# Optimization experiments

Measured on AMD Instinct MI355X. Metric: run time of the kernel, lower is better.

## Reference

```python
import jax, jax.numpy as jnp
import numpy as np

E = 512       # embed_dim
H = 8         # num_heads
DH = E // H   # head dim
F = 2048      # dim_feedforward
KS = 33       # NATTEN kernel_size (dilation=1)
NCLS = 1
B = 2
L = 4096      # local tokens (total seq = L + NCLS)
EPS = 1e-5


def layernorm(x, g, b):
    mu = jnp.mean(x, axis=-1, keepdims=True)
    var = jnp.mean(jnp.square(x - mu), axis=-1, keepdims=True)
    return (x - mu) * jax.lax.rsqrt(var + EPS) * g + b


def natten_1d(x, qkv_w, qkv_b, proj_w, proj_b):
    # Neighborhood attention 1D, dilation=1, non-causal, no rel-pos bias.
    b, l, e = x.shape
    qkv = x @ qkv_w.T + qkv_b                       # [b, l, 3E]
    q, k, v = jnp.split(qkv, 3, axis=-1)
    q = q.reshape(b, l, H, DH) * (DH ** -0.5)
    k = k.reshape(b, l, H, DH)
    v = v.reshape(b, l, H, DH)
    # NATTEN window: centered, shifted at edges to keep exactly KS in-bounds neighbors
    starts = jnp.clip(jnp.arange(l) - KS // 2, 0, l - KS)   # [l]
    idx = starts[:, None] + jnp.arange(KS)                  # [l, KS]
    kn = k[:, idx]                                          # [b, l, KS, H, DH]
    vn = v[:, idx]                                          # [b, l, KS, H, DH]
    attn = jnp.einsum('blhd,blkhd->bhlk', q, kn)
    attn = jax.nn.softmax(attn, axis=-1)
    out = jnp.einsum('bhlk,blkhd->blhd', attn, vn).reshape(b, l, e)
    return out @ proj_w.T + proj_b


def global_mha(q_in, kv_in, in_w, in_b, out_w, out_b):
    # torch nn.MultiheadAttention, batch_first, no masks
    bq, lq, e = q_in.shape
    lk = kv_in.shape[1]
    wq, wk, wv = jnp.split(in_w, 3, axis=0)
    bqp, bkp, bvp = jnp.split(in_b, 3, axis=0)
    q = (q_in @ wq.T + bqp).reshape(bq, lq, H, DH) * (DH ** -0.5)
    k = (kv_in @ wk.T + bkp).reshape(bq, lk, H, DH)
    v = (kv_in @ wv.T + bvp).reshape(bq, lk, H, DH)
    attn = jax.nn.softmax(jnp.einsum('bqhd,bkhd->bhqk', q, k), axis=-1)
    out = jnp.einsum('bhqk,bkhd->bqhd', attn, v).reshape(bq, lq, e)
    return out @ out_w.T + out_b


def setup_inputs() -> dict:
    key = jax.random.key(0)
    ks = jax.random.split(key, 16)
    s = 0.02
    return {
        'x': jax.random.normal(ks[0], (B, L + NCLS, E), jnp.float32),
        'ln1_g': jnp.ones((E,), jnp.float32),
        'ln1_b': jnp.zeros((E,), jnp.float32),
        'qkv_w': jax.random.normal(ks[1], (3 * E, E), jnp.float32) * s,
        'qkv_b': jnp.zeros((3 * E,), jnp.float32),
        'na_proj_w': jax.random.normal(ks[2], (E, E), jnp.float32) * s,
        'na_proj_b': jnp.zeros((E,), jnp.float32),
        'in_proj_w': jax.random.normal(ks[3], (3 * E, E), jnp.float32) * s,
        'in_proj_b': jnp.zeros((3 * E,), jnp.float32),
        'out_w': jax.random.normal(ks[4], (E, E), jnp.float32) * s,
        'out_b': jnp.zeros((E,), jnp.float32),
        'ln2_g': jnp.ones((E,), jnp.float32),
        'ln2_b': jnp.zeros((E,), jnp.float32),
        'fc1_w': jax.random.normal(ks[5], (F, E), jnp.float32) * s,
        'fc1_b': jnp.zeros((F,), jnp.float32),
        'fc2_w': jax.random.normal(ks[6], (E, F), jnp.float32) * s,
        'fc2_b': jnp.zeros((E,), jnp.float32),
    }


def reference(x, ln1_g, ln1_b, qkv_w, qkv_b, na_proj_w, na_proj_b,
              in_proj_w, in_proj_b, out_w, out_b, ln2_g, ln2_b,
              fc1_w, fc1_b, fc2_w, fc2_b):
    res = x
    xn = layernorm(x, ln1_g, ln1_b)
    x_local = natten_1d(xn[:, :-NCLS, :], qkv_w, qkv_b, na_proj_w, na_proj_b)
    tmp_key = jnp.concatenate([x_local, xn[:, -NCLS:, :]], axis=1)
    x_cls = global_mha(xn[:, -NCLS:, :], tmp_key, in_proj_w, in_proj_b, out_w, out_b)
    x = res + jnp.concatenate([x_local, x_cls], axis=1)
    res = x
    xn = layernorm(x, ln2_g, ln2_b)
    h = jax.nn.silu(xn @ fc1_w.T + fc1_b)
    return res + (h @ fc2_w.T + fc2_b)
```

## Files before the change

kernel.cpp:

```cpp
#include <hip/hip_runtime.h>
#include <hip/hip_bf16.h>
#include <cstdint>
#include <cstddef>

#define E    512
#define H    8
#define DHD  64
#define FDIM 2048
#define KS   33
#define BB   2
#define LL   4096
#define LP1  4097
#define NTOK 8194
#define NLOC 8192

typedef unsigned short ushort_t;
typedef __bf16 bf16x8_t __attribute__((ext_vector_type(8)));
typedef float  f32x4_t  __attribute__((ext_vector_type(4)));

__device__ __forceinline__ float b2f(unsigned short h) {
  union { unsigned int u; float f; } un; un.u = ((unsigned int)h) << 16; return un.f;
}
__device__ __forceinline__ unsigned short f2b(float f) {
  union { float f; unsigned int u; } un; un.f = f;
  unsigned int u = un.u;
  return (unsigned short)((u + 0x7FFFu + ((u >> 16) & 1u)) >> 16);
}

__device__ __forceinline__ void gload16(const ushort_t* g, ushort_t* l) {
  __builtin_amdgcn_global_load_lds(
      (const __attribute__((address_space(1))) void*)g,
      (__attribute__((address_space(3))) void*)l,
      16, 0, 0);
}

__device__ __forceinline__ int xcd_remap(int hw, int n) {
  int xcd = hw & 7, j = hw >> 3;
  int q = n >> 3, r = n & 7;
  return (xcd < r ? xcd * (q + 1) : r * (q + 1) + (xcd - r) * q) + j;
}

template<int BNT, int WC, int ACT, int OUTF, int ADDRES, int INRM, int OUTRM, int PARTIAL>
__global__ __launch_bounds__(256) void gemm_bt(
    const ushort_t* __restrict__ A, const ushort_t* __restrict__ W,
    const float* __restrict__ bias, float* __restrict__ outF,
    ushort_t* __restrict__ outB, const float* __restrict__ res,
    int M, int N, int K, int klen, int ny, int nz, size_t pstr)
{
  constexpr int MF = 4;
  constexpr int NF = BNT / (WC * 16);
  constexpr int BR = (BNT * 64) / (8 * 256);
  __shared__ ushort_t Alds[128 * 64];
  __shared__ ushort_t Blds[BNT * 64];
  const int t    = threadIdx.x;
  const int lane = t & 63;
  const int w    = t >> 6;
  const int wr   = w / WC, wc = w % WC;

  const int Lid = xcd_remap(blockIdx.x, gridDim.x);
  const int bx  = Lid / (ny * nz);
  const int rem = Lid % (ny * nz);
  const int z   = rem / ny;
  const int by  = rem % ny;
  const int bmBase = bx * 128;
  const int bnBase = by * BNT;
  const int kbeg = z * klen;

  f32x4_t zero = {0.f, 0.f, 0.f, 0.f};
  f32x4_t acc[MF][NF];
  #pragma unroll
  for (int m = 0; m < MF; ++m)
    #pragma unroll
    for (int n = 0; n < NF; ++n) acc[m][n] = zero;

  const int srow = t >> 3;
  const int jsw8 = ((t & 7) ^ (srow & 7)) * 8;
  int arow[4];
  #pragma unroll
  for (int r = 0; r < 4; ++r) {
    int rr = bmBase + r * 32 + srow;
    if (INRM) rr += rr >> 12;
    else if (rr >= M) rr = M - 1;
    arow[r] = rr;
  }
  int brow[BR];
  #pragma unroll
  for (int r = 0; r < BR; ++r) brow[r] = bnBase + r * 32 + srow;

  const int frow = lane & 15;
  const int g    = lane >> 4;

  for (int k0 = kbeg; k0 < kbeg + klen; k0 += 64) {
    #pragma unroll
    for (int r = 0; r < 4; ++r)
      gload16(A + (size_t)arow[r] * K + k0 + jsw8, &Alds[(size_t)(r * 256 + t) * 8]);
    #pragma unroll
    for (int r = 0; r < BR; ++r)
      gload16(W + (size_t)brow[r] * K + k0 + jsw8, &Blds[(size_t)(r * 256 + t) * 8]);
    __syncthreads();
    #pragma unroll
    for (int kk2 = 0; kk2 < 2; ++kk2) {
      bf16x8_t af[MF], bfv[NF];
      const int kosw = ((kk2 * 4 + g) ^ (frow & 7)) << 4;
      #pragma unroll
      for (int m = 0; m < MF; ++m) {
        int row = wr * 64 + m * 16 + frow;
        af[m] = *reinterpret_cast<const bf16x8_t*>((char*)Alds + row * 128 + kosw);
      }
      #pragma unroll
      for (int n = 0; n < NF; ++n) {
        int row = wc * (BNT / WC) + n * 16 + frow;
        bfv[n] = *reinterpret_cast<const bf16x8_t*>((char*)Blds + row * 128 + kosw);
      }
      __builtin_amdgcn_s_setprio(1);
      #pragma unroll
      for (int m = 0; m < MF; ++m)
        #pragma unroll
        for (int n = 0; n < NF; ++n)
          acc[m][n] = __builtin_amdgcn_mfma_f32_16x16x32_bf16(af[m], bfv[n], acc[m][n], 0, 0, 0);
      __builtin_amdgcn_s_setprio(0);
    }
    __syncthreads();
  }

  const int rbase = g * 4;
  const int cbase = frow;
  float* po = nullptr;
  if (PARTIAL) po = (z == nz - 1) ? (float*)outB : outF + (size_t)z * pstr;
  #pragma unroll
  for (int m = 0; m < MF; ++m) {
    #pragma unroll
    for (int r = 0; r < 4; ++r) {
      int gr = bmBase + wr * 64 + m * 16 + rbase + r;
      if (gr < M) {
        int orow = OUTRM ? gr + (gr >> 12) : gr;
        #pragma unroll
        for (int n = 0; n < NF; ++n) {
          int gc = bnBase + wc * (BNT / WC) + n * 16 + cbase;
          float v = acc[m][n][r];
          if (PARTIAL) {
            po[(size_t)orow * N + gc] = v;
          } else {
            v += bias[gc];
            if (ACT == 1) v = v / (1.f + __expf(-v));
            if (ADDRES) v += res[(size_t)gr * N + gc];
            if (OUTF) outF[(size_t)orow * N + gc] = v;
            else      outB[(size_t)orow * N + gc] = f2b(v);
          }
        }
      }
    }
  }
}

template<int NP>
__global__ __launch_bounds__(256) void fc2_reduce(
    float* __restrict__ out, const float* __restrict__ parts, size_t pstr4,
    const float* __restrict__ bias, const float* __restrict__ xa)
{
  size_t i = (size_t)blockIdx.x * 256 + threadIdx.x;
  float4 o = reinterpret_cast<const float4*>(out)[i];
  float4 x = reinterpret_cast<const float4*>(xa)[i];
  float4 bcol = reinterpret_cast<const float4*>(bias)[i & 127];
  o.x += x.x + bcol.x; o.y += x.y + bcol.y;
  o.z += x.z + bcol.z; o.w += x.w + bcol.w;
  #pragma unroll
  for (int zp = 0; zp < NP - 1; ++zp) {
    float4 a = reinterpret_cast<const float4*>(parts)[zp * pstr4 + i];
    o.x += a.x; o.y += a.y; o.z += a.z; o.w += a.w;
  }
  reinterpret_cast<float4*>(out)[i] = o;
}

__global__ __launch_bounds__(256) void ln_fused1(
    const float* __restrict__ x, const float* __restrict__ g,
    const float* __restrict__ be, ushort_t* __restrict__ xn,
    ushort_t* __restrict__ tmpk)
{
  __shared__ float sh[4];
  const int row = blockIdx.x;
  const int t = threadIdx.x;
  const float* xr = x + (size_t)row * E;
  float v0 = xr[t], v1 = xr[t + 256];
  float sum = v0 + v1;
  #pragma unroll
  for (int o = 32; o; o >>= 1) sum += __shfl_xor(sum, o);
  if ((t & 63) == 0) sh[t >> 6] = sum;
  __syncthreads();
  float mean = (sh[0] + sh[1] + sh[2] + sh[3]) * (1.f / E);
  __syncthreads();
  float d0 = v0 - mean, d1 = v1 - mean;
  float vs = d0 * d0 + d1 * d1;
  #pragma unroll
  for (int o = 32; o; o >>= 1) vs += __shfl_xor(vs, o);
  if ((t & 63) == 0) sh[t >> 6] = vs;
  __syncthreads();
  float var = (sh[0] + sh[1] + sh[2] + sh[3]) * (1.f / E);
  float rstd = rsqrtf(var + 1e-5f);
  unsigned short o0 = f2b(d0 * rstd * g[t] + be[t]);
  unsigned short o1 = f2b(d1 * rstd * g[t + 256] + be[t + 256]);
  xn[(size_t)row * E + t] = o0;
  xn[(size_t)row * E + t + 256] = o1;
  if ((row % LP1) == LL) {
    tmpk[(size_t)row * E + t] = o0;
    tmpk[(size_t)row * E + t + 256] = o1;
  }
}

__global__ __launch_bounds__(256) void resid_ln2(
    const float* __restrict__ x, const ushort_t* __restrict__ tmpk,
    const float* __restrict__ xcls, const float* __restrict__ g,
    const float* __restrict__ be, float* __restrict__ xa,
    ushort_t* __restrict__ xn2)
{
  __shared__ float sh[4];
  const int row = blockIdx.x;
  const int b = row / LP1, l = row % LP1;
  const int t = threadIdx.x;
  float a0, a1;
  if (l < LL) { a0 = b2f(tmpk[(size_t)row * E + t]); a1 = b2f(tmpk[(size_t)row * E + t + 256]); }
  else        { a0 = xcls[b * E + t];                a1 = xcls[b * E + t + 256]; }
  float v0 = x[(size_t)row * E + t] + a0;
  float v1 = x[(size_t)row * E + t + 256] + a1;
  xa[(size_t)row * E + t] = v0;
  xa[(size_t)row * E + t + 256] = v1;
  float sum = v0 + v1;
  #pragma unroll
  for (int o = 32; o; o >>= 1) sum += __shfl_xor(sum, o);
  if ((t & 63) == 0) sh[t >> 6] = sum;
  __syncthreads();
  float mean = (sh[0] + sh[1] + sh[2] + sh[3]) * (1.f / E);
  __syncthreads();
  float d0 = v0 - mean, d1 = v1 - mean;
  float vs = d0 * d0 + d1 * d1;
  #pragma unroll
  for (int o = 32; o; o >>= 1) vs += __shfl_xor(vs, o);
  if ((t & 63) == 0) sh[t >> 6] = vs;
  __syncthreads();
  float var = (sh[0] + sh[1] + sh[2] + sh[3]) * (1.f / E);
  float rstd = rsqrtf(var + 1e-5f);
  xn2[(size_t)row * E + t]       = f2b(d0 * rstd * g[t] + be[t]);
  xn2[(size_t)row * E + t + 256] = f2b(d1 * rstd * g[t + 256] + be[t + 256]);
}

__global__ __launch_bounds__(256) void natten_mfma(
    const ushort_t* __restrict__ qkv, ushort_t* __restrict__ out)
{
  __shared__ ushort_t KP[4][64 * 64];
  __shared__ ushort_t VT[4][64 * 72];
  const int w    = threadIdx.x >> 6;
  const int lane = threadIdx.x & 63;
  const int task = blockIdx.x * 4 + w;
  const int h  = task & 7;
  const int qb = (task >> 3) & 127;
  const int b  = task >> 10;
  const int l0 = qb * 32;
  const int kb = l0 - 16;
  const ushort_t* base = qkv + (size_t)b * LL * (3 * E);
  ushort_t* Klds = KP[w];
  ushort_t* Vt   = VT[w];

  {
    const int rsub = lane >> 3;
    const int d0   = (lane & 7) * 8;
    #pragma unroll
    for (int i = 0; i < 8; ++i) {
      int row = i * 8 + rsub;
      int gl = kb + row; gl = gl < 0 ? 0 : (gl > LL - 1 ? LL - 1 : gl);
      bf16x8_t kv = *reinterpret_cast<const bf16x8_t*>(
          base + (size_t)gl * (3 * E) + E + h * 64 + d0);
      int ba = (row * 128 + d0 * 2) ^ ((row & 7) << 4);
      *reinterpret_cast<bf16x8_t*>((char*)Klds + ba) = kv;
    }
  }
  {
    const int a  = lane & 7;
    const int c8 = lane >> 3;
    unsigned int* Vt32 = (unsigned int*)Vt;
    #pragma unroll
    for (int i = 0; i < 4; ++i) {
      int rp = i * 8 + c8;
      int g0 = kb + rp * 2;     g0 = g0 < 0 ? 0 : (g0 > LL - 1 ? LL - 1 : g0);
      int g1 = kb + rp * 2 + 1; g1 = g1 < 0 ? 0 : (g1 > LL - 1 ? LL - 1 : g1);
      const ushort_t* v0 = base + (size_t)g0 * (3 * E) + 2 * E + h * 64 + a * 8;
      const ushort_t* v1 = base + (size_t)g1 * (3 * E) + 2 * E + h * 64 + a * 8;
      ushort4 x0 = *(const ushort4*)v0,       x1 = *(const ushort4*)v1;
      ushort4 y0 = *(const ushort4*)(v0 + 4), y1 = *(const ushort4*)(v1 + 4);
      int d = a * 8;
      Vt32[(d + 0) * 36 + rp] = (unsigned)x0.x | ((unsigned)x1.x << 16);
      Vt32[(d + 1) * 36 + rp] = (unsigned)x0.y | ((unsigned)x1.y << 16);
      Vt32[(d + 2) * 36 + rp] = (unsigned)x0.z | ((unsigned)x1.z << 16);
      Vt32[(d + 3) * 36 + rp] = (unsigned)x0.w | ((unsigned)x1.w << 16);
      Vt32[(d + 4) * 36 + rp] = (unsigned)y0.x | ((unsigned)y1.x << 16);
      Vt32[(d + 5) * 36 + rp] = (unsigned)y0.y | ((unsigned)y1.y << 16);
      Vt32[(d + 6) * 36 + rp] = (unsigned)y0.z | ((unsigned)y1.z << 16);
      Vt32[(d + 7) * 36 + rp] = (unsigned)y0.w | ((unsigned)y1.w << 16);
    }
  }

  const int p = lane & 15, g = lane >> 4;
  bf16x8_t qf[2][2];
  #pragma unroll
  for (int mt = 0; mt < 2; ++mt)
    #pragma unroll
    for (int ks = 0; ks < 2; ++ks)
      qf[mt][ks] = *reinterpret_cast<const bf16x8_t*>(
          base + (size_t)(l0 + mt * 16 + p) * (3 * E) + h * 64 + ks * 32 + g * 8);

  f32x4_t zero = {0.f, 0.f, 0.f, 0.f};
  f32x4_t accS[2][4];
  #pragma unroll
  for (int mt = 0; mt < 2; ++mt)
    #pragma unroll
    for (int nt = 0; nt < 4; ++nt) accS[mt][nt] = zero;
  #pragma unroll
  for (int ks = 0; ks < 2; ++ks) {
    bf16x8_t kf[4];
    #pragma unroll
    for (int nt = 0; nt < 4; ++nt) {
      int row = nt * 16 + p;
      int ba = (row * 128 + (ks * 32 + g * 8) * 2) ^ ((row & 7) << 4);
      kf[nt] = *reinterpret_cast<const bf16x8_t*>((char*)Klds + ba);
    }
    #pragma unroll
    for (int mt = 0; mt < 2; ++mt)
      #pragma unroll
      for (int nt = 0; nt < 4; ++nt)
        accS[mt][nt] = __builtin_amdgcn_mfma_f32_16x16x32_bf16(qf[mt][ks], kf[nt], accS[mt][nt], 0, 0, 0);
  }

  ushort_t* Plds = Klds;
  #pragma unroll
  for (int mt = 0; mt < 2; ++mt) {
    #pragma unroll
    for (int r = 0; r < 4; ++r) {
      int lq = l0 + mt * 16 + g * 4 + r;
      int st = lq - 16; st = st < 0 ? 0 : (st > LL - KS ? LL - KS : st);
      int clo = st - kb, chi = clo + 32;
      float sv[4];
      float mx = -1e30f;
      #pragma unroll
      for (int nt = 0; nt < 4; ++nt) {
        int c = nt * 16 + p;
        float s = accS[mt][nt][r] * 0.125f;
        s = (c >= clo && c <= chi) ? s : -1e30f;
        sv[nt] = s;
        mx = fmaxf(mx, s);
      }
      mx = fmaxf(mx, __shfl_xor(mx, 1));
      mx = fmaxf(mx, __shfl_xor(mx, 2));
      mx = fmaxf(mx, __shfl_xor(mx, 4));
      mx = fmaxf(mx, __shfl_xor(mx, 8));
      float sum = 0.f;
      #pragma unroll
      for (int nt = 0; nt < 4; ++nt) { float e = __expf(sv[nt] - mx); sv[nt] = e; sum += e; }
      sum += __shfl_xor(sum, 1);
      sum += __shfl_xor(sum, 2);
      sum += __shfl_xor(sum, 4);
      sum += __shfl_xor(sum, 8);
      float inv = 1.f / sum;
      int q = mt * 16 + g * 4 + r;
      #pragma unroll
      for (int nt = 0; nt < 4; ++nt)
        Plds[q * 72 + nt * 16 + p] = f2b(sv[nt] * inv);
    }
  }

  f32x4_t accO[2][4];
  #pragma unroll
  for (int mt = 0; mt < 2; ++mt)
    #pragma unroll
    for (int nt = 0; nt < 4; ++nt) accO[mt][nt] = zero;
  #pragma unroll
  for (int ks = 0; ks < 2; ++ks) {
    bf16x8_t pf[2], vf[4];
    #pragma unroll
    for (int mt = 0; mt < 2; ++mt)
      pf[mt] = *reinterpret_cast<const bf16x8_t*>(
          (char*)Plds + (mt * 16 + p) * 144 + (ks * 32 + g * 8) * 2);
    #pragma unroll
    for (int nt = 0; nt < 4; ++nt)
      vf[nt] = *reinterpret_cast<const bf16x8_t*>(
          (char*)Vt + (nt * 16 + p) * 144 + (ks * 32 + g * 8) * 2);
    #pragma unroll
    for (int mt = 0; mt < 2; ++mt)
      #pragma unroll
      for (int nt = 0; nt < 4; ++nt)
        accO[mt][nt] = __builtin_amdgcn_mfma_f32_16x16x32_bf16(pf[mt], vf[nt], accO[mt][nt], 0, 0, 0);
  }

  #pragma unroll
  for (int mt = 0; mt < 2; ++mt) {
    #pragma unroll
    for (int r = 0; r < 4; ++r) {
      int lq = l0 + mt * 16 + g * 4 + r;
      ushort_t* orow = out + ((size_t)(b * LL) + lq) * E + h * 64;
      #pragma unroll
      for (int nt = 0; nt < 4; ++nt)
        orow[nt * 16 + p] = f2b(accO[mt][nt][r]);
    }
  }
}

__global__ __launch_bounds__(256) void qcls_kernel(
    const ushort_t* __restrict__ xn, const float* __restrict__ inw,
    const float* __restrict__ inb, float* __restrict__ qcls)
{
  int i = blockIdx.x * 256 + threadIdx.x;
  int b = i >> 9, d = i & 511;
  const ushort_t* xr = xn + ((size_t)b * LP1 + LL) * E;
  const float* wr = inw + (size_t)d * E;
  float s = 0.f;
  for (int e = 0; e < E; e += 4) {
    ushort4 xv = *reinterpret_cast<const ushort4*>(xr + e);
    s += b2f(xv.x) * wr[e] + b2f(xv.y) * wr[e + 1] + b2f(xv.z) * wr[e + 2] + b2f(xv.w) * wr[e + 3];
  }
  qcls[i] = (s + inb[d]) * 0.125f;
}

__global__ __launch_bounds__(256) void gscore_kernel(
    const float* __restrict__ qcls, const ushort_t* __restrict__ kv,
    float* __restrict__ sc)
{
  const int wav = blockIdx.x * 4 + (threadIdx.x >> 6);
  if (wav >= BB * LP1) return;
  const int lane = threadIdx.x & 63;
  const int b = wav / LP1, j = wav % LP1;
  const ushort_t* kr = kv + (size_t)wav * 1024 + lane * 8;
  const float* q = qcls + b * E + lane * 8;
  ushort4 ka = *reinterpret_cast<const ushort4*>(kr);
  ushort4 kb4 = *reinterpret_cast<const ushort4*>(kr + 4);
  float s = b2f(ka.x) * q[0] + b2f(ka.y) * q[1] + b2f(ka.z) * q[2] + b2f(ka.w) * q[3]
          + b2f(kb4.x) * q[4] + b2f(kb4.y) * q[5] + b2f(kb4.z) * q[6] + b2f(kb4.w) * q[7];
  s += __shfl_xor(s, 1); s += __shfl_xor(s, 2); s += __shfl_xor(s, 4);
  if ((lane & 7) == 0) sc[((size_t)(b * 8) + (lane >> 3)) * LP1 + j] = s;
}

__global__ __launch_bounds__(256) void gsoftmax_kernel(float* __restrict__ sc)
{
  float* row = sc + (size_t)blockIdx.x * LP1;
  __shared__ float sh[4];
  const int t = threadIdx.x;
  float m = -1e30f;
  for (int i = t; i < LP1; i += 256) m = fmaxf(m, row[i]);
  #pragma unroll
  for (int o = 32; o; o >>= 1) m = fmaxf(m, __shfl_xor(m, o));
  if ((t & 63) == 0) sh[t >> 6] = m;
  __syncthreads();
  m = fmaxf(fmaxf(sh[0], sh[1]), fmaxf(sh[2], sh[3]));
  __syncthreads();
  float s = 0.f;
  for (int i = t; i < LP1; i += 256) { float e = __expf(row[i] - m); row[i] = e; s += e; }
  #pragma unroll
  for (int o = 32; o; o >>= 1) s += __shfl_xor(s, o);
  if ((t & 63) == 0) sh[t >> 6] = s;
  __syncthreads();
  float inv = 1.f / (sh[0] + sh[1] + sh[2] + sh[3]);
  for (int i = t; i < LP1; i += 256) row[i] *= inv;
}

__global__ __launch_bounds__(256) void gpv_kernel(
    const float* __restrict__ sc, const ushort_t* __restrict__ kv,
    float* __restrict__ parts)
{
  __shared__ float red[4][64];
  const int bh = blockIdx.y;
  const int b = bh >> 3, h = bh & 7;
  const int c = blockIdx.x;
  const int lane = threadIdx.x & 63, s4 = threadIdx.x >> 6;
  const int j0 = c * 512;
  const int jend = (j0 + 512 < LP1) ? j0 + 512 : LP1;
  const float* prow = sc + (size_t)bh * LP1;
  const ushort_t* vbase = kv + (size_t)b * LP1 * 1024 + 512 + h * 64 + lane;
  float acc = 0.f;
  for (int j = j0 + s4; j < jend; j += 4)
    acc += prow[j] * b2f(vbase[(size_t)j * 1024]);
  red[s4][lane] = acc;
  __syncthreads();
  if (s4 == 0)
    parts[((size_t)c * 16 + bh) * 64 + lane] = red[0][lane] + red[1][lane] + red[2][lane] + red[3][lane];
}

__global__ void gpv_reduce(const float* __restrict__ parts, float* __restrict__ oc)
{
  int i = blockIdx.x * 256 + threadIdx.x;
  if (i < BB * E) {
    float s = 0.f;
    #pragma unroll
    for (int c = 0; c < 9; ++c) s += parts[c * 1024 + i];
    oc[i] = s;
  }
}

__global__ __launch_bounds__(256) void xcls_kernel(
    const float* __restrict__ oc, const float* __restrict__ ow,
    const float* __restrict__ ob, float* __restrict__ xc)
{
  int i = blockIdx.x * 256 + threadIdx.x;
  if (i >= BB * E) return;
  int b = i >> 9, n = i & 511;
  const float* o = oc + b * E;
  const float* wr = ow + (size_t)n * E;
  float s = ob[n];
  for (int m = 0; m < E; ++m) s += o[m] * wr[m];
  xc[i] = s;
}

__global__ void cvt_all(
    const float* __restrict__ s0, ushort_t* __restrict__ d0, int n0,
    const float* __restrict__ s1, ushort_t* __restrict__ d1, int n1,
    const float* __restrict__ s2, ushort_t* __restrict__ d2, int n2,
    const float* __restrict__ s3, ushort_t* __restrict__ d3, int n3,
    const float* __restrict__ s4, ushort_t* __restrict__ d4, int n4)
{
  int i = (blockIdx.x * 256 + threadIdx.x) * 4;
  const float* s; ushort_t* d;
  if (i < n0)                { s = s0; d = d0; }
  else if ((i -= n0) < n1)   { s = s1; d = d1; }
  else if ((i -= n1) < n2)   { s = s2; d = d2; }
  else if ((i -= n2) < n3)   { s = s3; d = d3; }
  else if ((i -= n3) < n4)   { s = s4; d = d4; }
  else return;
  float4 v = *reinterpret_cast<const float4*>(s + i);
  ushort4 o;
  o.x = f2b(v.x); o.y = f2b(v.y); o.z = f2b(v.z); o.w = f2b(v.w);
  *reinterpret_cast<ushort4*>(d + i) = o;
}

extern "C" void kernel_launch(void* const* d_in, const int* in_sizes, int n_in,
                              void* d_out, int out_size, void* d_ws, size_t ws_size,
                              hipStream_t stream)
{
  const float* x      = (const float*)d_in[0];
  const float* ln1_g  = (const float*)d_in[1];
  const float* ln1_b  = (const float*)d_in[2];
  const float* qkv_w  = (const float*)d_in[3];
  const float* qkv_b  = (const float*)d_in[4];
  const float* na_w   = (const float*)d_in[5];
  const float* na_b   = (const float*)d_in[6];
  const float* in_w   = (const float*)d_in[7];
  const float* in_b   = (const float*)d_in[8];
  const float* out_w  = (const float*)d_in[9];
  const float* out_b  = (const float*)d_in[10];
  const float* ln2_g  = (const float*)d_in[11];
  const float* ln2_b  = (const float*)d_in[12];
  const float* fc1_w  = (const float*)d_in[13];
  const float* fc1_b  = (const float*)d_in[14];
  const float* fc2_w  = (const float*)d_in[15];
  const float* fc2_b  = (const float*)d_in[16];
  float* out = (float*)d_out;

  char* pws = (char*)d_ws;
  size_t off = 0;
  auto alloc = [&](size_t bytes) {
    void* r = pws + off; off = (off + bytes + 255) & ~(size_t)255; return r;
  };
  ushort_t* w_qkv = (ushort_t*)alloc((size_t)3 * E * E * 2);
  ushort_t* w_na  = (ushort_t*)alloc((size_t)E * E * 2);
  ushort_t* w_in  = (ushort_t*)alloc((size_t)3 * E * E * 2);
  ushort_t* w_fc1 = (ushort_t*)alloc((size_t)FDIM * E * 2);
  ushort_t* w_fc2 = (ushort_t*)alloc((size_t)E * FDIM * 2);
  ushort_t* xn1   = (ushort_t*)alloc((size_t)NTOK * E * 2);
  char*     bigR  = (char*)alloc((size_t)NTOK * FDIM * 2);
  ushort_t* qkvb  = (ushort_t*)bigR;
  ushort_t* natt  = (ushort_t*)(bigR + (size_t)NLOC * 3 * E * 2);
  ushort_t* kvg   = (ushort_t*)bigR;
  ushort_t* hbuf  = (ushort_t*)bigR;
  ushort_t* tmpk  = (ushort_t*)alloc((size_t)NTOK * E * 2);
  float*    sc    = (float*)alloc((size_t)BB * H * LP1 * 4);
  float*    qcls  = (float*)alloc(1024 * 4);
  float*    parts = (float*)alloc(9 * 16 * 64 * 4);
  float*    oc    = (float*)alloc(1024 * 4);
  float*    xcls  = (float*)alloc(1024 * 4);
  float*    xa    = (float*)alloc((size_t)NTOK * E * 4);
  ushort_t* xn2   = xn1;
  const size_t PS = (size_t)NTOK * E;
  size_t off_save = off;
  float* sk = (float*)alloc(3 * PS * 4);
  int nsplit = 4;
  if (off > ws_size) {
    off = off_save;
    sk = (float*)alloc(PS * 4);
    nsplit = 2;
    if (off > ws_size) { off = off_save; nsplit = 1; }
  }

  cvt_all<<<3840, 256, 0, stream>>>(
      qkv_w, w_qkv, 3 * E * E,
      na_w,  w_na,  E * E,
      in_w,  w_in,  3 * E * E,
      fc1_w, w_fc1, FDIM * E,
      fc2_w, w_fc2, E * FDIM);

  ln_fused1<<<NTOK, 256, 0, stream>>>(x, ln1_g, ln1_b, xn1, tmpk);
  qcls_kernel<<<4, 256, 0, stream>>>(xn1, in_w, in_b, qcls);
  gemm_bt<128,2, 0,0,0,1,0,0><<<64 * 12, 256, 0, stream>>>(
      xn1, w_qkv, qkv_b, nullptr, qkvb, nullptr, NLOC, 3 * E, E, E, 12, 1, 0);
  natten_mfma<<<512, 256, 0, stream>>>(qkvb, natt);
  gemm_bt<64,2, 0,0,0,0,1,0><<<64 * 8, 256, 0, stream>>>(
      natt, w_na, na_b, nullptr, tmpk, nullptr, NLOC, E, E, E, 8, 1, 0);
  gemm_bt<128,2, 0,0,0,0,0,0><<<65 * 8, 256, 0, stream>>>(
      tmpk, w_in + (size_t)E * E, in_b + E, nullptr, kvg, nullptr, NTOK, 1024, E, E, 8, 1, 0);
  gscore_kernel<<<(BB * LP1 + 3) / 4, 256, 0, stream>>>(qcls, kvg, sc);
  gsoftmax_kernel<<<BB * H, 256, 0, stream>>>(sc);
  gpv_kernel<<<dim3(9, BB * H), 256, 0, stream>>>(sc, kvg, parts);
  gpv_reduce<<<4, 256, 0, stream>>>(parts, oc);
  xcls_kernel<<<4, 256, 0, stream>>>(oc, out_w, out_b, xcls);
  resid_ln2<<<NTOK, 256, 0, stream>>>(x, tmpk, xcls, ln2_g, ln2_b, xa, xn2);
  gemm_bt<128,2, 1,0,0,0,0,0><<<65 * 16, 256, 0, stream>>>(
      xn2, w_fc1, fc1_b, nullptr, hbuf, nullptr, NTOK, FDIM, E, E, 16, 1, 0);
  if (nsplit == 4) {
    gemm_bt<128,2, 0,0,0,0,0,1><<<65 * 4 * 4, 256, 0, stream>>>(
        hbuf, w_fc2, fc2_b, sk, (ushort_t*)out, nullptr, NTOK, E, FDIM, FDIM / 4, 4, 4, PS);
    fc2_reduce<4><<<(NTOK * E / 4) / 256, 256, 0, stream>>>(out, sk, PS / 4, fc2_b, xa);
  } else if (nsplit == 2) {
    gemm_bt<128,2, 0,0,0,0,0,1><<<65 * 4 * 2, 256, 0, stream>>>(
        hbuf, w_fc2, fc2_b, sk, (ushort_t*)out, nullptr, NTOK, E, FDIM, FDIM / 2, 4, 2, PS);
    fc2_reduce<2><<<(NTOK * E / 4) / 256, 256, 0, stream>>>(out, sk, PS / 4, fc2_b, xa);
  } else {
    gemm_bt<128,2, 0,1,1,0,0,0><<<65 * 4, 256, 0, stream>>>(
        hbuf, w_fc2, fc2_b, out, nullptr, xa, NTOK, E, FDIM, FDIM, 4, 1, 0);
  }
}
```

Measured before the change: 269.4 us.

## Double-buffer GEMM LDS tiles with async global-to-LDS prefetch

```diff
diff --git a/kernel.cpp b/kernel.cpp
--- a/kernel.cpp
+++ b/kernel.cpp
@@ -34,6 +34,12 @@
       16, 0, 0);
 }
 
+template<int N> __device__ __forceinline__ void waitcnt_vm() {
+  if constexpr (N == 8)      asm volatile("s_waitcnt vmcnt(8)" ::: "memory");
+  else if constexpr (N == 6) asm volatile("s_waitcnt vmcnt(6)" ::: "memory");
+  else                       asm volatile("s_waitcnt vmcnt(0)" ::: "memory");
+}
+
 __device__ __forceinline__ int xcd_remap(int hw, int n) {
   int xcd = hw & 7, j = hw >> 3;
   int q = n >> 3, r = n & 7;
@@ -47,11 +53,12 @@
     ushort_t* __restrict__ outB, const float* __restrict__ res,
     int M, int N, int K, int klen, int ny, int nz, size_t pstr)
 {
-  constexpr int MF = 4;
-  constexpr int NF = BNT / (WC * 16);
-  constexpr int BR = (BNT * 64) / (8 * 256);
-  __shared__ ushort_t Alds[128 * 64];
-  __shared__ ushort_t Blds[BNT * 64];
+  constexpr int MF  = 4;
+  constexpr int NF  = BNT / (WC * 16);
+  constexpr int BR  = (BNT * 64) / (8 * 256);
+  constexpr int NLD = 4 + BR;
+  __shared__ ushort_t Alds[2][128 * 64];
+  __shared__ ushort_t Blds[2][BNT * 64];
   const int t    = threadIdx.x;
   const int lane = t & 63;
   const int w    = t >> 6;
@@ -90,14 +97,24 @@
   const int frow = lane & 15;
   const int g    = lane >> 4;
 
-  for (int k0 = kbeg; k0 < kbeg + klen; k0 += 64) {
+  auto STAGE = [&](int s, int k0) {
     #pragma unroll
     for (int r = 0; r < 4; ++r)
-      gload16(A + (size_t)arow[r] * K + k0 + jsw8, &Alds[(size_t)(r * 256 + t) * 8]);
+      gload16(A + (size_t)arow[r] * K + k0 + jsw8, &Alds[s][(size_t)(r * 256 + t) * 8]);
     #pragma unroll
     for (int r = 0; r < BR; ++r)
-      gload16(W + (size_t)brow[r] * K + k0 + jsw8, &Blds[(size_t)(r * 256 + t) * 8]);
-    __syncthreads();
+      gload16(W + (size_t)brow[r] * K + k0 + jsw8, &Blds[s][(size_t)(r * 256 + t) * 8]);
+  };
+
+  const int nt = klen >> 6;
+  STAGE(0, kbeg);
+  if (nt > 1) STAGE(1, kbeg + 64);
+
+  for (int it = 0; it < nt; ++it) {
+    const int cur = it & 1;
+    if (it < nt - 1) waitcnt_vm<NLD>();
+    else             waitcnt_vm<0>();
+    __builtin_amdgcn_s_barrier();
     #pragma unroll
     for (int kk2 = 0; kk2 < 2; ++kk2) {
       bf16x8_t af[MF], bfv[NF];
@@ -105,12 +122,12 @@
       #pragma unroll
       for (int m = 0; m < MF; ++m) {
         int row = wr * 64 + m * 16 + frow;
-        af[m] = *reinterpret_cast<const bf16x8_t*>((char*)Alds + row * 128 + kosw);
+        af[m] = *reinterpret_cast<const bf16x8_t*>((char*)Alds[cur] + row * 128 + kosw);
       }
       #pragma unroll
       for (int n = 0; n < NF; ++n) {
         int row = wc * (BNT / WC) + n * 16 + frow;
-        bfv[n] = *reinterpret_cast<const bf16x8_t*>((char*)Blds + row * 128 + kosw);
+        bfv[n] = *reinterpret_cast<const bf16x8_t*>((char*)Blds[cur] + row * 128 + kosw);
       }
       __builtin_amdgcn_s_setprio(1);
       #pragma unroll
@@ -120,7 +137,8 @@
           acc[m][n] = __builtin_amdgcn_mfma_f32_16x16x32_bf16(af[m], bfv[n], acc[m][n], 0, 0, 0);
       __builtin_amdgcn_s_setprio(0);
     }
-    __syncthreads();
+    __builtin_amdgcn_s_barrier();
+    if (it + 2 < nt) STAGE(cur, kbeg + (it + 2) * 64);
   }
 
   const int rbase = g * 4;
```

Result: slower. 282.4 us (+4.9%).
